# Kernel tuning notes

Hardware: AMD Instinct MI355X
Metric: run time of the kernel (lower is better)

Reference implementation:

```python
import jax, jax.numpy as jnp
import numpy as np

L = 50000          # n_agents - 1 neighbors
OBS = 256          # input_shape[0]
ACT = 64           # output_shape
OTHER = 512        # input_shape[1]
HID = 64           # rnn_hidden_dim (forced by attn shape: 64 + cate_dim)
CATE = 32          # cate_dim


def setup_inputs() -> dict:
    key = jax.random.key(0)
    ks = jax.random.split(key, 16)
    s = 0.05
    return {
        "inputs": jax.random.normal(ks[0], (OBS,), jnp.float32),
        "act_idx": jax.random.normal(ks[1], (ACT,), jnp.float32),
        "other_inputs": jax.random.normal(ks[2], (L, OTHER), jnp.float32),
        # fc11: Linear(OBS+ACT, 64)
        "W11": jax.random.normal(ks[3], (HID, OBS + ACT), jnp.float32) * s,
        "b11": jax.random.normal(ks[4], (HID,), jnp.float32) * s,
        # fc12: Linear(OTHER, CATE)
        "W12": jax.random.normal(ks[5], (CATE, OTHER), jnp.float32) * s,
        "b12": jax.random.normal(ks[6], (CATE,), jnp.float32) * s,
        # attn: Linear(HID+CATE, 1)
        "Wa": jax.random.normal(ks[7], (1, HID + CATE), jnp.float32) * s,
        "ba": jax.random.normal(ks[8], (1,), jnp.float32) * s,
        # attn_out: Linear(CATE, CATE)
        "Wao": jax.random.normal(ks[9], (CATE, CATE), jnp.float32) * s,
        "bao": jax.random.normal(ks[10], (CATE,), jnp.float32) * s,
        # fc2: Linear(HID+CATE, HID)
        "W2": jax.random.normal(ks[11], (HID, HID + CATE), jnp.float32) * s,
        "b2": jax.random.normal(ks[12], (HID,), jnp.float32) * s,
        # fc3: Linear(HID, 1)
        "W3": jax.random.normal(ks[13], (1, HID), jnp.float32) * s,
        "b3": jax.random.normal(ks[14], (1,), jnp.float32) * s,
    }


def reference(inputs, act_idx, other_inputs, W11, b11, W12, b12, Wa, ba, Wao, bao, W2, b2, W3, b3):
    # cat obs with one-hot-style action index vector (dim 0 of 1D tensors)
    x_in = jnp.concatenate([inputs, act_idx])            # [OBS+ACT]
    input_x = W11 @ x_in + b11                           # [HID]

    # per-neighbor embedding (vectorized over the L neighbors)
    emb = other_inputs @ W12.T + b12                     # [L, CATE]

    # attention score attn(relu(cat(input_x, emb_i))); relu is elementwise,
    # so split the attn weight into the input_x part and the emb part.
    rx = jax.nn.relu(input_x)                            # [HID]
    re = jax.nn.relu(emb)                                # [L, CATE]
    w = rx @ Wa[0, :HID] + re @ Wa[0, HID:] + ba[0]      # [L]
    aw = jax.nn.softmax(w)                               # softmax over neighbors

    # attention-weighted mixture of neighbor embeddings
    mixed = aw @ emb                                     # [CATE]
    mixed = jax.nn.relu(mixed) @ Wao.T + bao             # attn_out

    # straight-through categorical (argmax one-hot, soft gradient)
    z_prob = jax.nn.softmax(mixed)                       # [CATE]
    samples = jax.nn.one_hot(jnp.argmax(z_prob), CATE, dtype=z_prob.dtype)
    one_hot_st = samples + (z_prob - jax.lax.stop_gradient(z_prob))

    x = jax.nn.relu(jnp.concatenate([input_x, one_hot_st]))  # [HID+CATE]
    h = jax.nn.relu(W2 @ x + b2)                             # [HID]
    r = W3 @ h + b3                                          # [1]
    return (r, samples)
```

## Files before the change

### kernel.cpp

```cpp
#include <hip/hip_runtime.h>

#define L_N    50000
#define K_DIM  512
#define GRID1  256
#define NGRP   3125
#define SB()   __builtin_amdgcn_sched_barrier(0)

typedef __attribute__((ext_vector_type(8))) short bf16x8;
typedef __attribute__((ext_vector_type(4))) float f32x4;

__device__ __forceinline__ void split8(float4 a, float4 b, bf16x8& hi, bf16x8& lo) {
    float v[8] = {a.x, a.y, a.z, a.w, b.x, b.y, b.z, b.w};
    #pragma unroll
    for (int j = 0; j < 8; ++j) {
        unsigned u  = __float_as_uint(v[j]);
        unsigned hb = u & 0xFFFF0000u;
        float    lf = v[j] - __uint_as_float(hb);
        hi[j] = (short)(hb >> 16);
        lo[j] = (short)(__float_as_uint(lf) >> 16);
    }
}

__global__ __launch_bounds__(1024) void k_part(
    const float* __restrict__ other,
    const float* __restrict__ W12,
    const float* __restrict__ b12,
    const float* __restrict__ Wa,
    float* __restrict__ ws)
{
    __shared__ short whi[16384];
    __shared__ short wlo[16384];
    __shared__ float sbuf[16][34];

    const int tid  = threadIdx.x;
    const int lane = tid & 63;
    const int wv   = tid >> 6;
    const int cl   = lane & 15;
    const int g    = lane >> 4;

    #pragma unroll
    for (int c2 = 0; c2 < 2; ++c2) {
        const int u  = tid + c2 * 1024;
        const int ch = u >> 6, r = u & 63;
        const float* wp = W12 + (size_t)ch * K_DIM + (r >> 2) * 32 + (r & 3) * 4;
        const float4 f0 = *(const float4*)wp;
        const float4 f1 = *(const float4*)(wp + 16);
        bf16x8 h8, l8; split8(f0, f1, h8, l8);
        const int p = (r * 32 + (ch ^ (r & 31))) * 8;
        *(bf16x8*)&whi[p] = h8;
        *(bf16x8*)&wlo[p] = l8;
    }
    __syncthreads();

    float rps = 0.f, rm0 = 0.f, rm1 = 0.f;
    const int wid = blockIdx.x * 16 + wv;

    if (wid < NGRP) {
        const float b0 = b12[cl],     b1 = b12[16 + cl];
        const float w0 = Wa[64 + cl], w1 = Wa[80 + cl];

        const float* xp = other + (size_t)(wid * 16 + cl) * K_DIM + (g << 2);

        float4 a0, a1, a2, a3, b0v, b1v, b2v, b3v, c0v, c1v, c2v, c3v, d0v, d1v, d2v, d3v;

        #define GLD(dst, OFF)                                                  \
            asm volatile("global_load_dwordx4 %0, %1, off offset:" OFF        \
                         : "=v"(dst) : "v"(xp) : "memory")
        #define GLDQ(x0,x1,x2,x3, O0,O1,O2,O3) do {                            \
            GLD(x0, O0); GLD(x1, O1); GLD(x2, O2); GLD(x3, O3);                \
        } while (0)
        #define VMW(N) do {                                                    \
            asm volatile("s_waitcnt vmcnt(" #N ")" ::: "memory");              \
            __builtin_amdgcn_sched_barrier(0);    \
        } while (0)

        f32x4 acc0 = {0.f,0.f,0.f,0.f}, acc1 = {0.f,0.f,0.f,0.f};

        #define CONSH(xlo, xhi, KC) do {                                       \
            bf16x8 ah, al; split8(xlo, xhi, ah, al);                           \
            const int r_  = (KC) * 4 + g;                                      \
            const int u0_ = (r_ * 32 + (cl ^ (r_ & 31))) * 8;                  \
            const bf16x8 bh0 = *(const bf16x8*)&whi[u0_];                      \
            const bf16x8 bl0 = *(const bf16x8*)&wlo[u0_];                      \
            const bf16x8 bh1 = *(const bf16x8*)&whi[u0_ ^ 128];                \
            const bf16x8 bl1 = *(const bf16x8*)&wlo[u0_ ^ 128];                \
            acc0 = __builtin_amdgcn_mfma_f32_16x16x32_bf16(ah, bh0, acc0, 0, 0, 0); \
            acc0 = __builtin_amdgcn_mfma_f32_16x16x32_bf16(al, bh0, acc0, 0, 0, 0); \
            acc0 = __builtin_amdgcn_mfma_f32_16x16x32_bf16(ah, bl0, acc0, 0, 0, 0); \
            acc1 = __builtin_amdgcn_mfma_f32_16x16x32_bf16(ah, bh1, acc1, 0, 0, 0); \
            acc1 = __builtin_amdgcn_mfma_f32_16x16x32_bf16(al, bh1, acc1, 0, 0, 0); \
            acc1 = __builtin_amdgcn_mfma_f32_16x16x32_bf16(ah, bl1, acc1, 0, 0, 0); \
        } while (0)
        #define CONSQ(x0,x1,x2,x3, QQ) do {                                    \
            CONSH(x0, x1, 2*(QQ));                                             \
            CONSH(x2, x3, 2*(QQ)+1);                                           \
        } while (0)

        GLDQ(a0,a1,a2,a3,   "0",   "64",  "128",  "192");
        GLDQ(b0v,b1v,b2v,b3v, "256",  "320",  "384",  "448");
        GLDQ(c0v,c1v,c2v,c3v, "512",  "576",  "640",  "704");
        GLDQ(d0v,d1v,d2v,d3v, "768",  "832",  "896",  "960");
        VMW(12); CONSQ(a0,a1,a2,a3, 0);  GLDQ(a0,a1,a2,a3, "1024","1088","1152","1216");
        VMW(12); CONSQ(b0v,b1v,b2v,b3v, 1); GLDQ(b0v,b1v,b2v,b3v, "1280","1344","1408","1472");
        VMW(12); CONSQ(c0v,c1v,c2v,c3v, 2); GLDQ(c0v,c1v,c2v,c3v, "1536","1600","1664","1728");
        VMW(12); CONSQ(d0v,d1v,d2v,d3v, 3); GLDQ(d0v,d1v,d2v,d3v, "1792","1856","1920","1984");
        VMW(12); CONSQ(a0,a1,a2,a3, 4);
        VMW(8);  CONSQ(b0v,b1v,b2v,b3v, 5);
        VMW(4);  CONSQ(c0v,c1v,c2v,c3v, 6);
        VMW(0);  CONSQ(d0v,d1v,d2v,d3v, 7);

        float e0[4], e1[4], s4[4];
        #pragma unroll
        for (int i = 0; i < 4; ++i) {
            e0[i] = acc0[i] + b0;
            e1[i] = acc1[i] + b1;
            s4[i] = fmaxf(e0[i], 0.f) * w0 + fmaxf(e1[i], 0.f) * w1;
        }
        #pragma unroll
        for (int d = 1; d < 16; d <<= 1) {
            #pragma unroll
            for (int i = 0; i < 4; ++i) s4[i] += __shfl_xor(s4[i], d);
        }
        #pragma unroll
        for (int i = 0; i < 4; ++i) {
            const float p = __expf(s4[i]);
            rps += p;
            rm0 = fmaf(p, e0[i], rm0);
            rm1 = fmaf(p, e1[i], rm1);
        }
    }

    rps += __shfl_xor(rps, 16); rps += __shfl_xor(rps, 32);
    rm0 += __shfl_xor(rm0, 16); rm0 += __shfl_xor(rm0, 32);
    rm1 += __shfl_xor(rm1, 16); rm1 += __shfl_xor(rm1, 32);
    if (lane == 0)  sbuf[wv][0] = rps;
    if (lane < 16) { sbuf[wv][1 + cl] = rm0; sbuf[wv][17 + cl] = rm1; }
    __syncthreads();
    if (wv == 0 && lane < 33) {
        float v = 0.f;
        #pragma unroll
        for (int s = 0; s < 16; ++s) v += sbuf[s][lane];
        ws[lane * GRID1 + blockIdx.x] = v;
    }
}

__global__ __launch_bounds__(256) void k_final(
    const float* __restrict__ ws,
    const float* __restrict__ inputs,
    const float* __restrict__ act_idx,
    const float* __restrict__ W11, const float* __restrict__ b11,
    const float* __restrict__ Wao, const float* __restrict__ bao,
    const float* __restrict__ W2,  const float* __restrict__ b2,
    const float* __restrict__ W3,  const float* __restrict__ b3,
    float* __restrict__ out)
{
    __shared__ float xsin[320];
    __shared__ float wsl[33];
    __shared__ float rm[32], z[32], xcat[96], h64[64];
    __shared__ int   amax;

    const int t = threadIdx.x, hh = t >> 2, q = t & 3;

    if (t < 132) {
        const int c = t >> 2, seg = t & 3;
        const float4* p = (const float4*)(ws + c * GRID1 + seg * 64);
        float v = 0.f;
        #pragma unroll
        for (int i = 0; i < 16; ++i) { const float4 f = p[i]; v += f.x + f.y + f.z + f.w; }
        v += __shfl_xor(v, 1);
        v += __shfl_xor(v, 2);
        if (seg == 0) wsl[c] = v;
    }
    xsin[t] = inputs[t];
    if (t < 64) xsin[256 + t] = act_idx[t];
    __syncthreads();

    if (t < 32) rm[t] = fmaxf(wsl[1 + t] / wsl[0], 0.f);

    float bp = 0.f;
    {
        const float4* wrow = (const float4*)(W11 + hh * 320 + q * 80);
        #pragma unroll
        for (int i = 0; i < 20; ++i) {
            const float4 f = wrow[i];
            const int k = q * 80 + i * 4;
            bp = fmaf(f.x, xsin[k], bp);
            bp = fmaf(f.y, xsin[k + 1], bp);
            bp = fmaf(f.z, xsin[k + 2], bp);
            bp = fmaf(f.w, xsin[k + 3], bp);
        }
    }
    bp += __shfl_xor(bp, 1);
    bp += __shfl_xor(bp, 2);
    __syncthreads();

    if (t < 32) {
        float zz = bao[t];
        for (int d = 0; d < 32; ++d) zz = fmaf(Wao[t * 32 + d], rm[d], zz);
        z[t] = zz;
    }
    __syncthreads();
    if (t == 0) {
        int bi = 0; float bv = z[0];
        for (int c = 1; c < 32; ++c) { if (z[c] > bv) { bv = z[c]; bi = c; } }
        amax = bi;
    }
    __syncthreads();
    if (q == 0) xcat[hh] = fmaxf(bp + b11[hh], 0.f);
    if (t < 32) xcat[64 + t] = (t == amax) ? 1.f : 0.f;
    __syncthreads();

    float dp = 0.f;
    for (int i = 0; i < 24; ++i) {
        const int k = q * 24 + i;
        dp = fmaf(W2[hh * 96 + k], xcat[k], dp);
    }
    dp += __shfl_xor(dp, 1);
    dp += __shfl_xor(dp, 2);
    if (q == 0) h64[hh] = fmaxf(dp + b2[hh], 0.f);
    __syncthreads();

    if (t == 0) {
        float r = b3[0];
        for (int i = 0; i < 64; ++i) r = fmaf(W3[i], h64[i], r);
        out[0] = r;
    }
    if (t < 32) out[1 + t] = (t == amax) ? 1.f : 0.f;
}

extern "C" void kernel_launch(void* const* d_in, const int* in_sizes, int n_in,
                              void* d_out, int out_size, void* d_ws, size_t ws_size,
                              hipStream_t stream) {
    const float* inputs  = (const float*)d_in[0];
    const float* act_idx = (const float*)d_in[1];
    const float* other   = (const float*)d_in[2];
    const float* W11     = (const float*)d_in[3];
    const float* b11     = (const float*)d_in[4];
    const float* W12     = (const float*)d_in[5];
    const float* b12     = (const float*)d_in[6];
    const float* Wa      = (const float*)d_in[7];
    const float* Wao     = (const float*)d_in[9];
    const float* bao     = (const float*)d_in[10];
    const float* W2      = (const float*)d_in[11];
    const float* b2      = (const float*)d_in[12];
    const float* W3      = (const float*)d_in[13];
    const float* b3      = (const float*)d_in[14];
    float* ws = (float*)d_ws;

    k_part<<<GRID1, 1024, 0, stream>>>(other, W12, b12, Wa, ws);
    k_final<<<1, 256, 0, stream>>>(ws, inputs, act_idx, W11, b11,
                                   Wao, bao, W2, b2, W3, b3, (float*)d_out);
}
```

Measured before the change: 32.33 us.

## Interleave wave-to-group mapping across blocks and parallelize tail reductions with shuffles

Changes the mapping of waves to row groups so consecutive groups are spread across blocks rather than packed within one block, which balances load when the group count does not divide evenly. In the final single-block kernel, the attn_out matvec, the argmax and the fc3 dot product are parallelized with warp shuffles instead of serial per-thread loops. These aim to shorten the serial tail and even out work in the main pass. The argmax tie-breaking keeps the lowest index, matching the previous serial scan.

```diff
diff --git a/kernel.cpp b/kernel.cpp
--- a/kernel.cpp
+++ b/kernel.cpp
@@ -53,7 +53,8 @@
     __syncthreads();
 
     float rps = 0.f, rm0 = 0.f, rm1 = 0.f;
-    const int wid = blockIdx.x * 16 + wv;
+
+    const int wid = wv * GRID1 + blockIdx.x;
 
     if (wid < NGRP) {
         const float b0 = b12[cl],     b1 = b12[16 + cl];
@@ -71,7 +72,7 @@
         } while (0)
         #define VMW(N) do {                                                    \
             asm volatile("s_waitcnt vmcnt(" #N ")" ::: "memory");              \
-            __builtin_amdgcn_sched_barrier(0);    \
+            __builtin_amdgcn_sched_barrier(0);                    \
         } while (0)
 
         f32x4 acc0 = {0.f,0.f,0.f,0.f}, acc1 = {0.f,0.f,0.f,0.f};
@@ -194,16 +195,27 @@
     bp += __shfl_xor(bp, 2);
     __syncthreads();
 
+    {
+        const int o = t >> 3, kb = (t & 7) * 4;
+        float zz = 0.f;
+        #pragma unroll
+        for (int j = 0; j < 4; ++j) zz = fmaf(Wao[o * 32 + kb + j], rm[kb + j], zz);
+        zz += __shfl_xor(zz, 1);
+        zz += __shfl_xor(zz, 2);
+        zz += __shfl_xor(zz, 4);
+        if ((t & 7) == 0) z[o] = zz + bao[o];
+    }
+    __syncthreads();
+
     if (t < 32) {
-        float zz = bao[t];
-        for (int d = 0; d < 32; ++d) zz = fmaf(Wao[t * 32 + d], rm[d], zz);
-        z[t] = zz;
-    }
-    __syncthreads();
-    if (t == 0) {
-        int bi = 0; float bv = z[0];
-        for (int c = 1; c < 32; ++c) { if (z[c] > bv) { bv = z[c]; bi = c; } }
-        amax = bi;
+        float bv = z[t]; int bi = t;
+        #pragma unroll
+        for (int d = 1; d < 32; d <<= 1) {
+            const float ov = __shfl_xor(bv, d);
+            const int   oi = __shfl_xor(bi, d);
+            if (ov > bv || (ov == bv && oi < bi)) { bv = ov; bi = oi; }
+        }
+        if (t == 0) amax = bi;
     }
     __syncthreads();
     if (q == 0) xcat[hh] = fmaxf(bp + b11[hh], 0.f);
@@ -220,10 +232,11 @@
     if (q == 0) h64[hh] = fmaxf(dp + b2[hh], 0.f);
     __syncthreads();
 
-    if (t == 0) {
-        float r = b3[0];
-        for (int i = 0; i < 64; ++i) r = fmaf(W3[i], h64[i], r);
-        out[0] = r;
+    if (t < 64) {
+        float r = W3[t] * h64[t];
+        #pragma unroll
+        for (int d = 1; d < 64; d <<= 1) r += __shfl_xor(r, d);
+        if (t == 0) out[0] = r + b3[0];
     }
     if (t < 32) out[1 + t] = (t == amax) ? 1.f : 0.f;
 }
```

Result: slower. 33.15 us (+2.5%).
